# Kernel tuning notes

Measured on AMD Instinct MI355X. Metric: run time of the kernel, lower is better.

## Reference

```python
import jax, jax.numpy as jnp
import numpy as np


def setup_inputs() -> dict:
    key = jax.random.key(0)
    k1, k2, k3, k4, k5 = jax.random.split(key, 5)
    B, T, H = 32, 4096, 256
    D = 2 * H  # encoder feature dim
    hidden = jax.random.normal(k1, (B, D), dtype=jnp.float32)
    encoder_outputs = jax.random.normal(k2, (B, T, D), dtype=jnp.float32)
    # torch nn.Linear(4H, H): weight [H, 4H], bias [H]
    W_attn = jax.random.normal(k3, (H, 4 * H), dtype=jnp.float32) * (1.0 / np.sqrt(4 * H))
    b_attn = jax.random.normal(k4, (H,), dtype=jnp.float32) * 0.01
    v = jax.random.uniform(k5, (H,), dtype=jnp.float32)  # torch.rand init
    return {"hidden": hidden, "encoder_outputs": encoder_outputs,
            "W_attn": W_attn, "b_attn": b_attn, "v": v}


def reference(hidden, encoder_outputs, W_attn, b_attn, v):
    D = hidden.shape[-1]  # 2*H
    # Split Linear(4H->H) weight into the hidden part and encoder part so we
    # never materialize the [B,T,4H] concat: cat(h,e) @ W.T == h @ Wh.T + e @ We.T
    W_h = W_attn[:, :D]   # [H, 2H]
    W_e = W_attn[:, D:]   # [H, 2H]
    h_proj = hidden @ W_h.T                     # [B, H]
    e_proj = jnp.einsum('btd,hd->bth', encoder_outputs, W_e)  # [B, T, H]
    energy = jnp.tanh(h_proj[:, None, :] + e_proj + b_attn)   # [B, T, H]
    scores = energy @ v                          # [B, T]
    attn_weights = jax.nn.softmax(scores, axis=1)  # softmax over timesteps
    context = jnp.einsum('bt,btd->bd', attn_weights, encoder_outputs)  # [B, 2H]
    return context, attn_weights
```

## Files before the change

kernel.cpp:

```cpp
#include <hip/hip_runtime.h>
#include <math.h>

#define B_  32
#define T_  4096
#define H_  256
#define D_  512

#define WS_PRE    0
#define WS_WEHI   32768
#define WS_SCORES 557056

using short8  = __attribute__((ext_vector_type(8))) short;
using float4v = __attribute__((ext_vector_type(4))) float;

__device__ __forceinline__ unsigned short f32_to_bf16_rne(float x) {
    unsigned u = __float_as_uint(x);
    unsigned r = u + 0x7fffu + ((u >> 16) & 1u);
    return (unsigned short)(r >> 16);
}

__global__ __launch_bounds__(256)
void prep_kernel(const float* __restrict__ hidden,
                 const float* __restrict__ W_attn,
                 const float* __restrict__ b_attn,
                 unsigned char* __restrict__ ws,
                 float* __restrict__ out_ctx) {
    int blk = blockIdx.x;
    int tid = threadIdx.x;
    if (blk < 32) {
        int b = blk, h = tid;
        const float4* hv = (const float4*)(hidden + b * D_);
        const float4* wv = (const float4*)(W_attn + (size_t)h * 1024);
        float s = 0.f;
        #pragma unroll 4
        for (int d4 = 0; d4 < D_ / 4; ++d4) {
            float4 a = hv[d4], w = wv[d4];
            s += a.x * w.x + a.y * w.y + a.z * w.z + a.w * w.w;
        }
        ((float*)(ws + WS_PRE))[b * H_ + h] = s + b_attn[h];
    } else if (blk < 40) {
        int base = (blk - 32) * 16384 + tid;
        unsigned short* whi = (unsigned short*)(ws + WS_WEHI);
        #pragma unroll 4
        for (int i = 0; i < 64; ++i) {
            int idx = base + i * 256;
            int n = idx >> 9, k = idx & 511;
            whi[idx] = f32_to_bf16_rne(W_attn[(size_t)n * 1024 + 512 + k]);
        }
    } else {
        for (int i = tid; i < B_ * D_; i += 256) out_ctx[i] = 0.f;
    }
}

#define BM 128
#define BN 256
#define BK 32
#define LDT 40

__global__ __launch_bounds__(512, 4)
void gemm_scores_kernel(const float* __restrict__ enc,
                        const unsigned char* __restrict__ ws_ro,
                        const float* __restrict__ v,
                        float* __restrict__ scores_out) {
    __shared__ unsigned short sA[2][BM * LDT];
    __shared__ unsigned short sB[2][BN * LDT];
    __shared__ float sScore[BM];

    const float*          pre = (const float*)(ws_ro + WS_PRE);
    const unsigned short* weh = (const unsigned short*)(ws_ro + WS_WEHI);

    int tid = threadIdx.x;
    int m0  = blockIdx.x * BM;
    int b   = m0 >> 12;

    if (tid < BM) sScore[tid] = 0.f;

    int rowA = tid & 127, cgA = tid >> 7;
    const float* gA = enc + (size_t)(m0 + rowA) * D_ + cgA * 8;
    int rowB = tid >> 1, hB = tid & 1;
    const unsigned short* gB = weh + (size_t)rowB * D_ + hB * 16;

    int wave = tid >> 6, lane = tid & 63;
    int wm = wave & 1, wn = wave >> 1;
    int quad = lane >> 4, l16 = lane & 15;

    float4v acc[4][4] = {};

    float a_reg[8];
    uint4 br0, br1;

    {
        const float4* p = (const float4*)gA;
        *(float4*)(a_reg)     = p[0];
        *(float4*)(a_reg + 4) = p[1];
        br0 = ((const uint4*)gB)[0]; br1 = ((const uint4*)gB)[1];

        unsigned short hi8[8];
        #pragma unroll
        for (int j = 0; j < 8; ++j) hi8[j] = f32_to_bf16_rne(a_reg[j]);
        *(short8*)&sA[0][rowA * LDT + cgA * 8] = *(short8*)hi8;
        *(uint4*)&sB[0][rowB * LDT + hB * 16]     = br0;
        *(uint4*)&sB[0][rowB * LDT + hB * 16 + 8] = br1;

        const float4* p1 = (const float4*)(gA + BK);
        *(float4*)(a_reg)     = p1[0];
        *(float4*)(a_reg + 4) = p1[1];
        const uint4* pb1 = (const uint4*)(gB + BK);
        br0 = pb1[0]; br1 = pb1[1];
    }
    __builtin_amdgcn_s_waitcnt(0xc07f);
    __builtin_amdgcn_s_barrier();

    const int KIT = D_ / BK;
    for (int kk = 0; kk < KIT; ++kk) {
        int cur = kk & 1, nxt = cur ^ 1;

        short8 ah[4], bh[4];
        #pragma unroll
        for (int i = 0; i < 4; ++i) {
            int r = wm * 64 + i * 16 + l16;
            ah[i] = *(const short8*)&sA[cur][r * LDT + quad * 8];
        }
        #pragma unroll
        for (int j = 0; j < 4; ++j) {
            int c = wn * 64 + j * 16 + l16;
            bh[j] = *(const short8*)&sB[cur][c * LDT + quad * 8];
        }

        if (kk + 1 < KIT) {
            unsigned short hi8[8];
            #pragma unroll
            for (int j = 0; j < 8; ++j) hi8[j] = f32_to_bf16_rne(a_reg[j]);
            *(short8*)&sA[nxt][rowA * LDT + cgA * 8] = *(short8*)hi8;
            *(uint4*)&sB[nxt][rowB * LDT + hB * 16]     = br0;
            *(uint4*)&sB[nxt][rowB * LDT + hB * 16 + 8] = br1;
        }
        if (kk + 2 < KIT) {
            const float4* p = (const float4*)(gA + (kk + 2) * BK);
            *(float4*)(a_reg)     = p[0];
            *(float4*)(a_reg + 4) = p[1];
            const uint4* pb = (const uint4*)(gB + (kk + 2) * BK);
            br0 = pb[0]; br1 = pb[1];
        }

        #pragma unroll
        for (int i = 0; i < 4; ++i)
            #pragma unroll
            for (int j = 0; j < 4; ++j)
                acc[i][j] = __builtin_amdgcn_mfma_f32_16x16x32_bf16(ah[i], bh[j], acc[i][j], 0, 0, 0);

        if (kk + 1 < KIT) {
            __builtin_amdgcn_s_waitcnt(0xc07f);
            __builtin_amdgcn_s_barrier();
        }
    }

    float rowsum[4][4] = {};
    #pragma unroll
    for (int j = 0; j < 4; ++j) {
        int n = wn * 64 + j * 16 + l16;
        float pv = pre[b * H_ + n];
        float vv = v[n];
        #pragma unroll
        for (int i = 0; i < 4; ++i)
            #pragma unroll
            for (int r = 0; r < 4; ++r)
                rowsum[i][r] += tanhf(acc[i][j][r] + pv) * vv;
    }
    #pragma unroll
    for (int i = 0; i < 4; ++i)
        #pragma unroll
        for (int r = 0; r < 4; ++r) {
            float s = rowsum[i][r];
            s += __shfl_xor(s, 1);
            s += __shfl_xor(s, 2);
            s += __shfl_xor(s, 4);
            s += __shfl_xor(s, 8);
            rowsum[i][r] = s;
        }
    if (l16 == 0) {
        #pragma unroll
        for (int i = 0; i < 4; ++i)
            #pragma unroll
            for (int r = 0; r < 4; ++r) {
                int row = wm * 64 + i * 16 + quad * 4 + r;
                atomicAdd(&sScore[row], rowsum[i][r]);
            }
    }
    __syncthreads();
    if (tid < BM) scores_out[m0 + tid] = sScore[tid];
}

__global__ __launch_bounds__(1024)
void softmax_kernel(const float* __restrict__ scores, float* __restrict__ wout) {
    __shared__ float red[16];
    int b = blockIdx.x, tid = threadIdx.x;
    int wave = tid >> 6, lane = tid & 63;
    float4 x = ((const float4*)(scores + (size_t)b * T_))[tid];

    float m = fmaxf(fmaxf(x.x, x.y), fmaxf(x.z, x.w));
    #pragma unroll
    for (int off = 32; off; off >>= 1) m = fmaxf(m, __shfl_xor(m, off));
    if (lane == 0) red[wave] = m;
    __syncthreads();
    if (wave == 0) {
        float t = (lane < 16) ? red[lane] : -1e30f;
        #pragma unroll
        for (int off = 8; off; off >>= 1) t = fmaxf(t, __shfl_xor(t, off));
        if (lane == 0) red[0] = t;
    }
    __syncthreads();
    m = red[0];
    __syncthreads();

    float4 e;
    e.x = expf(x.x - m); e.y = expf(x.y - m);
    e.z = expf(x.z - m); e.w = expf(x.w - m);
    float s = e.x + e.y + e.z + e.w;
    #pragma unroll
    for (int off = 32; off; off >>= 1) s += __shfl_xor(s, off);
    if (lane == 0) red[wave] = s;
    __syncthreads();
    if (wave == 0) {
        float t = (lane < 16) ? red[lane] : 0.f;
        #pragma unroll
        for (int off = 8; off; off >>= 1) t += __shfl_xor(t, off);
        if (lane == 0) red[0] = t;
    }
    __syncthreads();
    float inv = 1.0f / red[0];

    float4 o;
    o.x = e.x * inv; o.y = e.y * inv; o.z = e.z * inv; o.w = e.w * inv;
    ((float4*)(wout + (size_t)b * T_))[tid] = o;
}

__global__ __launch_bounds__(256)
void context_kernel(const float* __restrict__ enc,
                    const float* __restrict__ w,
                    float* __restrict__ ctx) {
    int blk = blockIdx.x;
    int b = blk >> 6, chunk = blk & 63;
    int tid = threadIdx.x;
    int colg = tid & 127, rh = tid >> 7;
    const float* encb = enc + (size_t)b * T_ * D_;
    int t0 = chunk * 64;

    float4 acc = {0.f, 0.f, 0.f, 0.f};
    #pragma unroll 8
    for (int s = 0; s < 32; ++s) {
        int t = t0 + rh + 2 * s;
        float wt = w[(size_t)b * T_ + t];
        float4 ev = *(const float4*)(encb + (size_t)t * D_ + colg * 4);
        acc.x += wt * ev.x; acc.y += wt * ev.y;
        acc.z += wt * ev.z; acc.w += wt * ev.w;
    }
    __shared__ float4 sred[128];
    if (rh == 1) sred[colg] = acc;
    __syncthreads();
    if (rh == 0) {
        float4 o = sred[colg];
        acc.x += o.x; acc.y += o.y; acc.z += o.z; acc.w += o.w;
        float* dst = ctx + (size_t)b * D_ + colg * 4;
        atomicAdd(dst + 0, acc.x);
        atomicAdd(dst + 1, acc.y);
        atomicAdd(dst + 2, acc.z);
        atomicAdd(dst + 3, acc.w);
    }
}

extern "C" void kernel_launch(void* const* d_in, const int* in_sizes, int n_in,
                              void* d_out, int out_size, void* d_ws, size_t ws_size,
                              hipStream_t stream) {
    const float* hidden = (const float*)d_in[0];
    const float* enc    = (const float*)d_in[1];
    const float* W_attn = (const float*)d_in[2];
    const float* b_attn = (const float*)d_in[3];
    const float* v      = (const float*)d_in[4];
    float* out = (float*)d_out;
    unsigned char* ws = (unsigned char*)d_ws;
    float* scores = (float*)(ws + WS_SCORES);

    prep_kernel<<<41, 256, 0, stream>>>(hidden, W_attn, b_attn, ws, out);
    gemm_scores_kernel<<<T_ * B_ / BM, 512, 0, stream>>>(enc, ws, v, scores);
    softmax_kernel<<<B_, 1024, 0, stream>>>(scores, out + B_ * D_);
    context_kernel<<<B_ * 64, 256, 0, stream>>>(enc, out + B_ * D_, out);
}
```

Measured before the change: 460.2 us.

## Fuse softmax and context into GEMM epilogue with split-softmax partials

The GEMM kernel's epilogue now computes per-tile local softmax statistics (max and sum). It writes unnormalized exponentials and computes a partial context vector from the encoder rows the tile just processed. A small finalize kernel then merges the per-tile max/sum and rescales both the attention weights and the partial contexts. This drops the separate softmax and context kernels, the second full pass over the encoder from DRAM, and the atomic accumulation. The trade-off is extra epilogue work and possible register/LDS pressure in the GEMM kernel.

```diff
diff --git a/kernel.cpp b/kernel.cpp
--- a/kernel.cpp
+++ b/kernel.cpp
@@ -8,7 +8,9 @@
 
 #define WS_PRE    0
 #define WS_WEHI   32768
-#define WS_SCORES 557056
+#define WS_P      294912
+#define WS_ML     819200
+#define WS_PCTX   827392
 
 using short8  = __attribute__((ext_vector_type(8))) short;
 using float4v = __attribute__((ext_vector_type(4))) float;
@@ -23,8 +25,7 @@
 void prep_kernel(const float* __restrict__ hidden,
                  const float* __restrict__ W_attn,
                  const float* __restrict__ b_attn,
-                 unsigned char* __restrict__ ws,
-                 float* __restrict__ out_ctx) {
+                 unsigned char* __restrict__ ws) {
     int blk = blockIdx.x;
     int tid = threadIdx.x;
     if (blk < 32) {
@@ -38,7 +39,7 @@
             s += a.x * w.x + a.y * w.y + a.z * w.z + a.w * w.w;
         }
         ((float*)(ws + WS_PRE))[b * H_ + h] = s + b_attn[h];
-    } else if (blk < 40) {
+    } else {
         int base = (blk - 32) * 16384 + tid;
         unsigned short* whi = (unsigned short*)(ws + WS_WEHI);
         #pragma unroll 4
@@ -47,8 +48,6 @@
             int n = idx >> 9, k = idx & 511;
             whi[idx] = f32_to_bf16_rne(W_attn[(size_t)n * 1024 + 512 + k]);
         }
-    } else {
-        for (int i = tid; i < B_ * D_; i += 256) out_ctx[i] = 0.f;
     }
 }
 
@@ -59,15 +58,16 @@
 
 __global__ __launch_bounds__(512, 4)
 void gemm_scores_kernel(const float* __restrict__ enc,
-                        const unsigned char* __restrict__ ws_ro,
-                        const float* __restrict__ v,
-                        float* __restrict__ scores_out) {
+                        unsigned char* __restrict__ ws,
+                        const float* __restrict__ v) {
     __shared__ unsigned short sA[2][BM * LDT];
     __shared__ unsigned short sB[2][BN * LDT];
     __shared__ float sScore[BM];
-
-    const float*          pre = (const float*)(ws_ro + WS_PRE);
-    const unsigned short* weh = (const unsigned short*)(ws_ro + WS_WEHI);
+    __shared__ float sP[BM];
+    __shared__ float sRed[4];
+
+    const float*          pre = (const float*)(ws + WS_PRE);
+    const unsigned short* weh = (const unsigned short*)(ws + WS_WEHI);
 
     int tid = threadIdx.x;
     int m0  = blockIdx.x * BM;
@@ -188,84 +188,95 @@
             }
     }
     __syncthreads();
-    if (tid < BM) scores_out[m0 + tid] = sScore[tid];
-}
-
-__global__ __launch_bounds__(1024)
-void softmax_kernel(const float* __restrict__ scores, float* __restrict__ wout) {
-    __shared__ float red[16];
+
+    if (tid < 128) {
+        float s = sScore[tid];
+        float m = s;
+        #pragma unroll
+        for (int off = 32; off; off >>= 1) m = fmaxf(m, __shfl_xor(m, off));
+        if (lane == 0) sRed[wave] = m;
+    }
+    __syncthreads();
+    float m_blk = fmaxf(sRed[0], sRed[1]);
+    if (tid < 128) {
+        float p = expf(sScore[tid] - m_blk);
+        sP[tid] = p;
+        ((float*)(ws + WS_P))[m0 + tid] = p;
+        float l = p;
+        #pragma unroll
+        for (int off = 32; off; off >>= 1) l += __shfl_xor(l, off);
+        if (lane == 0) sRed[2 + wave] = l;
+    }
+    __syncthreads();
+    if (tid == 0) {
+        float2 ml = make_float2(m_blk, sRed[2] + sRed[3]);
+        ((float2*)(ws + WS_ML))[blockIdx.x] = ml;
+    }
+
+    int colg = tid & 127, rgrp = tid >> 7;
+    const float* encb = enc + (size_t)m0 * D_;
+    float4 c4 = {0.f, 0.f, 0.f, 0.f};
+    #pragma unroll 4
+    for (int s = 0; s < 32; ++s) {
+        int r = rgrp + 4 * s;
+        float w = sP[r];
+        float4 ev = *(const float4*)(encb + (size_t)r * D_ + colg * 4);
+        c4.x += w * ev.x; c4.y += w * ev.y;
+        c4.z += w * ev.z; c4.w += w * ev.w;
+    }
+    float4* red4 = (float4*)sA;
+    red4[tid] = c4;
+    __syncthreads();
+    if (rgrp == 0) {
+        float4 a0 = red4[colg], a1 = red4[colg + 128];
+        float4 a2 = red4[colg + 256], a3 = red4[colg + 384];
+        float4 o;
+        o.x = a0.x + a1.x + a2.x + a3.x;
+        o.y = a0.y + a1.y + a2.y + a3.y;
+        o.z = a0.z + a1.z + a2.z + a3.z;
+        o.w = a0.w + a1.w + a2.w + a3.w;
+        ((float4*)(ws + WS_PCTX))[blockIdx.x * 128 + colg] = o;
+    }
+}
+
+__global__ __launch_bounds__(512)
+void finalize_kernel(const unsigned char* __restrict__ ws,
+                     float* __restrict__ out_ctx,
+                     float* __restrict__ out_w) {
+    __shared__ float sm[32], sl[32], sscale[32];
     int b = blockIdx.x, tid = threadIdx.x;
-    int wave = tid >> 6, lane = tid & 63;
-    float4 x = ((const float4*)(scores + (size_t)b * T_))[tid];
-
-    float m = fmaxf(fmaxf(x.x, x.y), fmaxf(x.z, x.w));
-    #pragma unroll
-    for (int off = 32; off; off >>= 1) m = fmaxf(m, __shfl_xor(m, off));
-    if (lane == 0) red[wave] = m;
-    __syncthreads();
-    if (wave == 0) {
-        float t = (lane < 16) ? red[lane] : -1e30f;
-        #pragma unroll
-        for (int off = 8; off; off >>= 1) t = fmaxf(t, __shfl_xor(t, off));
-        if (lane == 0) red[0] = t;
-    }
-    __syncthreads();
-    m = red[0];
-    __syncthreads();
-
-    float4 e;
-    e.x = expf(x.x - m); e.y = expf(x.y - m);
-    e.z = expf(x.z - m); e.w = expf(x.w - m);
-    float s = e.x + e.y + e.z + e.w;
-    #pragma unroll
-    for (int off = 32; off; off >>= 1) s += __shfl_xor(s, off);
-    if (lane == 0) red[wave] = s;
-    __syncthreads();
-    if (wave == 0) {
-        float t = (lane < 16) ? red[lane] : 0.f;
-        #pragma unroll
-        for (int off = 8; off; off >>= 1) t += __shfl_xor(t, off);
-        if (lane == 0) red[0] = t;
-    }
-    __syncthreads();
-    float inv = 1.0f / red[0];
-
-    float4 o;
-    o.x = e.x * inv; o.y = e.y * inv; o.z = e.z * inv; o.w = e.w * inv;
-    ((float4*)(wout + (size_t)b * T_))[tid] = o;
-}
-
-__global__ __launch_bounds__(256)
-void context_kernel(const float* __restrict__ enc,
-                    const float* __restrict__ w,
-                    float* __restrict__ ctx) {
-    int blk = blockIdx.x;
-    int b = blk >> 6, chunk = blk & 63;
-    int tid = threadIdx.x;
-    int colg = tid & 127, rh = tid >> 7;
-    const float* encb = enc + (size_t)b * T_ * D_;
-    int t0 = chunk * 64;
-
-    float4 acc = {0.f, 0.f, 0.f, 0.f};
-    #pragma unroll 8
-    for (int s = 0; s < 32; ++s) {
-        int t = t0 + rh + 2 * s;
-        float wt = w[(size_t)b * T_ + t];
-        float4 ev = *(const float4*)(encb + (size_t)t * D_ + colg * 4);
-        acc.x += wt * ev.x; acc.y += wt * ev.y;
-        acc.z += wt * ev.z; acc.w += wt * ev.w;
-    }
-    __shared__ float4 sred[128];
-    if (rh == 1) sred[colg] = acc;
-    __syncthreads();
-    if (rh == 0) {
-        float4 o = sred[colg];
-        acc.x += o.x; acc.y += o.y; acc.z += o.z; acc.w += o.w;
-        float* dst = ctx + (size_t)b * D_ + colg * 4;
-        atomicAdd(dst + 0, acc.x);
-        atomicAdd(dst + 1, acc.y);
-        atomicAdd(dst + 2, acc.z);
-        atomicAdd(dst + 3, acc.w);
+    const float2* ml  = ((const float2*)(ws + WS_ML)) + b * 32;
+    if (tid < 32) {
+        float2 v = ml[tid];
+        sm[tid] = v.x; sl[tid] = v.y;
+    }
+    __syncthreads();
+    float m = -1e30f;
+    #pragma unroll
+    for (int i = 0; i < 32; ++i) m = fmaxf(m, sm[i]);
+    float l = 0.f;
+    #pragma unroll
+    for (int i = 0; i < 32; ++i) l += sl[i] * expf(sm[i] - m);
+    float inv = 1.0f / l;
+    if (tid < 32) sscale[tid] = expf(sm[tid] - m) * inv;
+    __syncthreads();
+
+    {
+        const float4* pb = (const float4*)((const float*)(ws + WS_P) + (size_t)b * T_);
+        float4* wb = (float4*)(out_w + (size_t)b * T_);
+        int t0 = tid * 2;
+        float sc = sscale[tid >> 4];
+        float4 x = pb[t0], y = pb[t0 + 1];
+        x.x *= sc; x.y *= sc; x.z *= sc; x.w *= sc;
+        y.x *= sc; y.y *= sc; y.z *= sc; y.w *= sc;
+        wb[t0] = x; wb[t0 + 1] = y;
+    }
+    {
+        const float* pc = (const float*)(ws + WS_PCTX) + (size_t)b * 32 * D_;
+        float c = 0.f;
+        #pragma unroll
+        for (int i = 0; i < 32; ++i) c += pc[i * D_ + tid] * sscale[i];
+        out_ctx[b * D_ + tid] = c;
     }
 }
 
@@ -279,10 +290,8 @@
     const float* v      = (const float*)d_in[4];
     float* out = (float*)d_out;
     unsigned char* ws = (unsigned char*)d_ws;
-    float* scores = (float*)(ws + WS_SCORES);
-
-    prep_kernel<<<41, 256, 0, stream>>>(hidden, W_attn, b_attn, ws, out);
-    gemm_scores_kernel<<<T_ * B_ / BM, 512, 0, stream>>>(enc, ws, v, scores);
-    softmax_kernel<<<B_, 1024, 0, stream>>>(scores, out + B_ * D_);
-    context_kernel<<<B_ * 64, 256, 0, stream>>>(enc, out + B_ * D_, out);
-}
+
+    prep_kernel<<<40, 256, 0, stream>>>(hidden, W_attn, b_attn, ws);
+    gemm_scores_kernel<<<T_ * B_ / BM, 512, 0, stream>>>(enc, ws, v);
+    finalize_kernel<<<B_, 512, 0, stream>>>(ws, out, out + B_ * D_);
+}
```

Measured after the change: 439.3 us. -4.6%, faster.
